# Performance work log

Hardware: AMD Instinct MI355X
Metric: run time of the kernel (lower is better)

## Reference

```python
import jax, jax.numpy as jnp
import numpy as np

D_IN = 768
D_OUT = 768
NUM_HEADS = 12
HEAD_DIM = D_OUT // NUM_HEADS


def setup_inputs() -> dict:
    key = jax.random.key(0)
    ks = jax.random.split(key, 6)
    s = 0.02
    x = jax.random.normal(ks[0], (4, 1024, D_IN), dtype=jnp.float32)
    # torch Linear weights are [out_features, in_features]
    Wq = jax.random.normal(ks[1], (D_OUT, D_IN), dtype=jnp.float32) * s
    Wk = jax.random.normal(ks[2], (D_OUT, D_IN), dtype=jnp.float32) * s
    Wv = jax.random.normal(ks[3], (D_OUT, D_IN), dtype=jnp.float32) * s
    Wo = jax.random.normal(ks[4], (D_OUT, D_OUT), dtype=jnp.float32) * s
    bo = jax.random.normal(ks[5], (D_OUT,), dtype=jnp.float32) * s
    return {"x": x, "Wq": Wq, "Wk": Wk, "Wv": Wv, "Wo": Wo, "bo": bo}


def reference(x, Wq, Wk, Wv, Wo, bo):
    B, T, _ = x.shape
    H, Dh = NUM_HEADS, HEAD_DIM
    # QKV projections (no bias), reshape to [B, H, T, Dh]
    q = (x @ Wq.T).reshape(B, T, H, Dh).transpose(0, 2, 1, 3)
    k = (x @ Wk.T).reshape(B, T, H, Dh).transpose(0, 2, 1, 3)
    v = (x @ Wv.T).reshape(B, T, H, Dh).transpose(0, 2, 1, 3)
    # Scores [B, H, T, T]. NOTE: original torch code's masked_fill and dropout
    # are not in-place / not assigned, so neither affects the output.
    scores = jnp.einsum("bhqd,bhkd->bhqk", q, k)
    attn = jax.nn.softmax(scores / np.sqrt(Dh).astype(np.float32), axis=-1)
    ctx = jnp.einsum("bhqk,bhkd->bhqd", attn, v)
    ctx = ctx.transpose(0, 2, 1, 3).reshape(B, T, H * Dh)
    return ctx @ Wo.T + bo
```

## Files before the change

### kernel.cpp

```cpp
#include <hip/hip_runtime.h>

typedef _Float16 half8 __attribute__((ext_vector_type(8)));
typedef float f32x4 __attribute__((ext_vector_type(4)));
typedef unsigned short u16;

#define NHEAD 12
#define DHEAD 64
#define DM    768
#define TSEQ  1024

static constexpr size_t OFF_XH  = 0;
static constexpr size_t OFF_WQH = 3145728;
static constexpr size_t OFF_WKH = 3735552;
static constexpr size_t OFF_WVH = 4325376;
static constexpr size_t OFF_WOH = 4915200;
static constexpr size_t OFF_Q   = 5505024;
static constexpr size_t OFF_K   = 8650752;
static constexpr size_t OFF_VT  = 11796480;
static constexpr size_t OFF_CTX = 0;

typedef const __attribute__((address_space(1))) void* gas_ptr;
typedef __attribute__((address_space(3))) void* las_ptr;
__device__ __forceinline__ void gload16(const _Float16* g, _Float16* l) {
    __builtin_amdgcn_global_load_lds((gas_ptr)g, (las_ptr)l, 16, 0, 0);
}

__global__ void cvt_kernel(const float* __restrict__ x, const float* __restrict__ wq,
                           const float* __restrict__ wk, const float* __restrict__ wv,
                           const float* __restrict__ wo, _Float16* __restrict__ ws) {
    int seg = blockIdx.y;
    const float* src;
    _Float16* dst;
    int n;
    if (seg == 0)      { src = x;  dst = ws + OFF_XH;  n = 3145728; }
    else if (seg == 1) { src = wq; dst = ws + OFF_WQH; n = 589824; }
    else if (seg == 2) { src = wk; dst = ws + OFF_WKH; n = 589824; }
    else if (seg == 3) { src = wv; dst = ws + OFF_WVH; n = 589824; }
    else               { src = wo; dst = ws + OFF_WOH; n = 589824; }
    int i = (blockIdx.x * blockDim.x + threadIdx.x) * 8;
    if (i < n) {
        float4 v0 = *(const float4*)(src + i);
        float4 v1 = *(const float4*)(src + i + 4);
        half8 o;
        o[0] = (_Float16)v0.x; o[1] = (_Float16)v0.y;
        o[2] = (_Float16)v0.z; o[3] = (_Float16)v0.w;
        o[4] = (_Float16)v1.x; o[5] = (_Float16)v1.y;
        o[6] = (_Float16)v1.z; o[7] = (_Float16)v1.w;
        *(half8*)(dst + i) = o;
    }
}

__global__ __launch_bounds__(256) void qkv_kernel(_Float16* __restrict__ ws) {
    __shared__ __align__(16) _Float16 ldsA[128 * 32];
    __shared__ __align__(16) _Float16 ldsB[128 * 32];

    const int z = blockIdx.z;
    const _Float16* __restrict__ xh = ws + OFF_XH;
    const _Float16* __restrict__ w  = ws + (z == 0 ? OFF_WQH : z == 1 ? OFF_WKH : OFF_WVH);
    _Float16* __restrict__ outp     = ws + (z == 0 ? OFF_Q   : z == 1 ? OFF_K   : OFF_VT);

    const int tid  = threadIdx.x;
    const int lane = tid & 63;
    const int wid  = tid >> 6;
    const int quad = lane >> 4, l15 = lane & 15;
    const int wm = (wid & 1) * 64, wn = (wid >> 1) * 64;

    int mb, nb;
    const _Float16 *gA, *gB;
    if (z < 2) {
        mb = blockIdx.x * 128;
        nb = blockIdx.y * 128;
        gA = xh + (size_t)mb * DM;
        gB = w  + (size_t)nb * DM;
    } else {
        mb = blockIdx.y * 128;
        nb = blockIdx.x * 128;
        gA = w  + (size_t)mb * DM;
        gB = xh + (size_t)nb * DM;
    }

    const int srow = (lane >> 2);
    const int scol = (lane & 3) * 8;
    const size_t goff0 = (size_t)(wid * 32 + srow) * DM + scol;
    const size_t goff1 = (size_t)(wid * 32 + 16 + srow) * DM + scol;
    _Float16* lA0 = ldsA + wid * 1024;
    _Float16* lA1 = ldsA + wid * 1024 + 512;
    _Float16* lB0 = ldsB + wid * 1024;
    _Float16* lB1 = ldsB + wid * 1024 + 512;

    f32x4 acc[4][4] = {};
    for (int k0 = 0; k0 < DM; k0 += 32) {
        gload16(gA + goff0 + k0, lA0);
        gload16(gA + goff1 + k0, lA1);
        gload16(gB + goff0 + k0, lB0);
        gload16(gB + goff1 + k0, lB1);
        __syncthreads();

        half8 a[4], b[4];
#pragma unroll
        for (int t = 0; t < 4; t++) {
            a[t] = *(const half8*)(ldsA + (wm + t * 16 + l15) * 32 + quad * 8);
            b[t] = *(const half8*)(ldsB + (wn + t * 16 + l15) * 32 + quad * 8);
        }
#pragma unroll
        for (int mt = 0; mt < 4; mt++)
#pragma unroll
            for (int nt = 0; nt < 4; nt++)
                acc[mt][nt] = __builtin_amdgcn_mfma_f32_16x16x32_f16(a[mt], b[nt], acc[mt][nt], 0, 0, 0);
        __syncthreads();
    }

#pragma unroll
    for (int mt = 0; mt < 4; mt++)
#pragma unroll
        for (int nt = 0; nt < 4; nt++)
#pragma unroll
            for (int r = 0; r < 4; r++) {
                int m = mb + wm + mt * 16 + quad * 4 + r;
                int n = nb + wn + nt * 16 + l15;
                size_t idx;
                if (z < 2) {
                    int bb = m >> 10, tt = m & 1023;
                    int h = n >> 6, d = n & 63;
                    idx = ((size_t)(bb * NHEAD + h) * TSEQ + tt) * DHEAD + d;
                } else {
                    int h = m >> 6, d = m & 63;
                    int bb = n >> 10, tt = n & 1023;
                    idx = ((size_t)(bb * NHEAD + h) * DHEAD + d) * TSEQ + tt;
                }
                outp[idx] = (_Float16)acc[mt][nt][r];
            }
}

__global__ __launch_bounds__(256, 3) void attn_kernel(_Float16* __restrict__ ws) {
    __shared__ __align__(16) _Float16 ldsK[64 * 64];
    __shared__ __align__(16) _Float16 ldsV[64 * 64];
    __shared__ __align__(16) _Float16 ldsP[4][16 * 72];

    const int tid  = threadIdx.x;
    const int lane = tid & 63;
    const int wid  = tid >> 6;
    const int quad = lane >> 4, l15 = lane & 15;
    const int bh = blockIdx.y;
    const int q0 = blockIdx.x * 64 + wid * 16;

    const _Float16* __restrict__ Q  = ws + OFF_Q  + (size_t)bh * TSEQ * DHEAD;
    const _Float16* __restrict__ K  = ws + OFF_K  + (size_t)bh * TSEQ * DHEAD;
    const _Float16* __restrict__ VT = ws + OFF_VT + (size_t)bh * DHEAD * TSEQ;
    _Float16* __restrict__ ctx = ws + OFF_CTX;
    _Float16* pbase = ldsP[wid];

    const int srow0 = tid >> 3, sc0 = tid & 7;
    const int ldsOff0 = srow0 * 64 + ((sc0 ^ (srow0 & 7)) * 8);
    const int ldsOff1 = (srow0 + 32) * 64 + ((sc0 ^ (srow0 & 7)) * 8);

    half8 qf[2];
#pragma unroll
    for (int ks = 0; ks < 2; ks++)
        qf[ks] = *(const half8*)(Q + (size_t)(q0 + l15) * DHEAD + ks * 32 + quad * 8);

    float mrun[4], lrun[4];
    f32x4 oacc[4] = {};
#pragma unroll
    for (int r = 0; r < 4; r++) { mrun[r] = -1e30f; lrun[r] = 0.f; }

    uint4 ka, kb, va, vb;
    ka = *(const uint4*)(K + tid * 8);
    kb = *(const uint4*)(K + 2048 + tid * 8);
    va = *(const uint4*)(VT + (size_t)srow0 * TSEQ + sc0 * 8);
    vb = *(const uint4*)(VT + (size_t)(srow0 + 32) * TSEQ + sc0 * 8);

    for (int kt = 0; kt < TSEQ; kt += 64) {
        *(uint4*)(ldsK + ldsOff0) = ka;
        *(uint4*)(ldsK + ldsOff1) = kb;
        *(uint4*)(ldsV + ldsOff0) = va;
        *(uint4*)(ldsV + ldsOff1) = vb;
        __syncthreads();

        if (kt + 64 < TSEQ) {
            ka = *(const uint4*)(K + (kt + 64) * DHEAD + tid * 8);
            kb = *(const uint4*)(K + (kt + 64) * DHEAD + 2048 + tid * 8);
            va = *(const uint4*)(VT + (size_t)srow0 * TSEQ + kt + 64 + sc0 * 8);
            vb = *(const uint4*)(VT + (size_t)(srow0 + 32) * TSEQ + kt + 64 + sc0 * 8);
        }

        half8 kf[4][2];
#pragma unroll
        for (int n = 0; n < 4; n++)
#pragma unroll
            for (int ks = 0; ks < 2; ks++) {
                int row = n * 16 + l15;
                int phys = (ks * 4 + quad) ^ (row & 7);
                kf[n][ks] = *(const half8*)(ldsK + row * 64 + phys * 8);
            }

        f32x4 s[4] = {};
#pragma unroll
        for (int n = 0; n < 4; n++)
#pragma unroll
            for (int ks = 0; ks < 2; ks++)
                s[n] = __builtin_amdgcn_mfma_f32_16x16x32_f16(qf[ks], kf[n][ks], s[n], 0, 0, 0);
#pragma unroll
        for (int n = 0; n < 4; n++) s[n] *= 0.125f;

#pragma unroll
        for (int r = 0; r < 4; r++) {
            float tm = fmaxf(fmaxf(s[0][r], s[1][r]), fmaxf(s[2][r], s[3][r]));
#pragma unroll
            for (int off = 1; off < 16; off <<= 1) tm = fmaxf(tm, __shfl_xor(tm, off, 64));
            float mnew = fmaxf(mrun[r], tm);
            float alpha = __expf(mrun[r] - mnew);
            mrun[r] = mnew;
            float ts = 0.f;
#pragma unroll
            for (int n = 0; n < 4; n++) {
                float e = __expf(s[n][r] - mnew);
                s[n][r] = e;
                ts += e;
            }
#pragma unroll
            for (int off = 1; off < 16; off <<= 1) ts += __shfl_xor(ts, off, 64);
            lrun[r] = lrun[r] * alpha + ts;
#pragma unroll
            for (int dn = 0; dn < 4; dn++) oacc[dn][r] *= alpha;
        }

#pragma unroll
        for (int n = 0; n < 4; n++)
#pragma unroll
            for (int r = 0; r < 4; r++)
                pbase[(quad * 4 + r) * 72 + n * 16 + l15] = (_Float16)s[n][r];

        half8 vf[4][2];
#pragma unroll
        for (int dn = 0; dn < 4; dn++)
#pragma unroll
            for (int ks = 0; ks < 2; ks++) {
                int row = dn * 16 + l15;
                int phys = (ks * 4 + quad) ^ (row & 7);
                vf[dn][ks] = *(const half8*)(ldsV + row * 64 + phys * 8);
            }

        half8 pf[2];
#pragma unroll
        for (int ks = 0; ks < 2; ks++)
            pf[ks] = *(const half8*)(pbase + l15 * 72 + ks * 32 + quad * 8);

#pragma unroll
        for (int dn = 0; dn < 4; dn++)
#pragma unroll
            for (int ks = 0; ks < 2; ks++)
                oacc[dn] = __builtin_amdgcn_mfma_f32_16x16x32_f16(pf[ks], vf[dn][ks], oacc[dn], 0, 0, 0);

        __syncthreads();
    }

    const int b_ = bh / NHEAD, h = bh % NHEAD;
#pragma unroll
    for (int dn = 0; dn < 4; dn++)
#pragma unroll
        for (int r = 0; r < 4; r++) {
            int t_ = q0 + quad * 4 + r;
            int col = h * DHEAD + dn * 16 + l15;
            float v = oacc[dn][r] / lrun[r];
            ctx[((size_t)(b_ * TSEQ + t_)) * DM + col] = (_Float16)v;
        }
}

__global__ __launch_bounds__(256) void proj_kernel(const _Float16* __restrict__ ws,
                                                   const float* __restrict__ bo,
                                                   float* __restrict__ out) {
    __shared__ __align__(16) _Float16 ldsA[128 * 32];
    __shared__ __align__(16) _Float16 ldsB[128 * 32];

    const _Float16* __restrict__ gA = ws + OFF_CTX + (size_t)blockIdx.x * 128 * DM;
    const _Float16* __restrict__ gB = ws + OFF_WOH + (size_t)blockIdx.y * 128 * DM;

    const int tid  = threadIdx.x;
    const int lane = tid & 63;
    const int wid  = tid >> 6;
    const int quad = lane >> 4, l15 = lane & 15;
    const int wm = (wid & 1) * 64, wn = (wid >> 1) * 64;

    const int srow = (lane >> 2);
    const int scol = (lane & 3) * 8;
    const size_t goff0 = (size_t)(wid * 32 + srow) * DM + scol;
    const size_t goff1 = (size_t)(wid * 32 + 16 + srow) * DM + scol;
    _Float16* lA0 = ldsA + wid * 1024;
    _Float16* lA1 = ldsA + wid * 1024 + 512;
    _Float16* lB0 = ldsB + wid * 1024;
    _Float16* lB1 = ldsB + wid * 1024 + 512;

    f32x4 acc[4][4] = {};
    for (int k0 = 0; k0 < DM; k0 += 32) {
        gload16(gA + goff0 + k0, lA0);
        gload16(gA + goff1 + k0, lA1);
        gload16(gB + goff0 + k0, lB0);
        gload16(gB + goff1 + k0, lB1);
        __syncthreads();

        half8 a[4], b[4];
#pragma unroll
        for (int t = 0; t < 4; t++) {
            a[t] = *(const half8*)(ldsA + (wm + t * 16 + l15) * 32 + quad * 8);
            b[t] = *(const half8*)(ldsB + (wn + t * 16 + l15) * 32 + quad * 8);
        }
#pragma unroll
        for (int mt = 0; mt < 4; mt++)
#pragma unroll
            for (int nt = 0; nt < 4; nt++)
                acc[mt][nt] = __builtin_amdgcn_mfma_f32_16x16x32_f16(a[mt], b[nt], acc[mt][nt], 0, 0, 0);
        __syncthreads();
    }

    const int mb = blockIdx.x * 128, nb = blockIdx.y * 128;
#pragma unroll
    for (int mt = 0; mt < 4; mt++)
#pragma unroll
        for (int nt = 0; nt < 4; nt++)
#pragma unroll
            for (int r = 0; r < 4; r++) {
                int m = mb + wm + mt * 16 + quad * 4 + r;
                int n = nb + wn + nt * 16 + l15;
                out[(size_t)m * DM + n] = acc[mt][nt][r] + bo[n];
            }
}

extern "C" void kernel_launch(void* const* d_in, const int* in_sizes, int n_in,
                              void* d_out, int out_size, void* d_ws, size_t ws_size,
                              hipStream_t stream) {
    const float* x  = (const float*)d_in[0];
    const float* wq = (const float*)d_in[1];
    const float* wk = (const float*)d_in[2];
    const float* wv = (const float*)d_in[3];
    const float* wo = (const float*)d_in[4];
    const float* bo = (const float*)d_in[5];
    _Float16* ws = (_Float16*)d_ws;
    float* out = (float*)d_out;

    cvt_kernel<<<dim3(1536, 5, 1), 256, 0, stream>>>(x, wq, wk, wv, wo, ws);
    qkv_kernel<<<dim3(32, 6, 3), 256, 0, stream>>>(ws);
    attn_kernel<<<dim3(16, 48, 1), 256, 0, stream>>>(ws);
    proj_kernel<<<dim3(32, 6, 1), 256, 0, stream>>>(ws, bo, out);
}
```

Baseline: 160.8 us.

## Split attention over the key dimension with a combine kernel, use exp2 softmax

Adds a split-K flash-attention path that divides the 1024 keys into two halves across blockIdx.z. It writes unnormalized fp16 partial outputs plus per-row max and sum to the workspace, and a new combine kernel merges them into ctx. This doubles the grid to raise occupancy and parallelism (768 to 1536 blocks), at the cost of an extra launch and extra global traffic. It also folds the 1/sqrt(d) scale into Q in fp16 and replaces __expf with exp2 plus an FMA. The split path runs only when the workspace is large enough.

```diff
diff --git a/kernel.cpp b/kernel.cpp
--- a/kernel.cpp
+++ b/kernel.cpp
@@ -8,6 +8,7 @@
 #define DHEAD 64
 #define DM    768
 #define TSEQ  1024
+#define LOG2E 1.44269504f
 
 static constexpr size_t OFF_XH  = 0;
 static constexpr size_t OFF_WQH = 3145728;
@@ -18,6 +19,9 @@
 static constexpr size_t OFF_K   = 8650752;
 static constexpr size_t OFF_VT  = 11796480;
 static constexpr size_t OFF_CTX = 0;
+static constexpr size_t OFF_OP  = 14942208;
+static constexpr size_t OFF_ML_BYTES = 42467328;
+static constexpr size_t WS_NEED_SPLITK = 43253760;
 
 typedef const __attribute__((address_space(1))) void* gas_ptr;
 typedef __attribute__((address_space(3))) void* las_ptr;
@@ -132,7 +136,8 @@
             }
 }
 
-__global__ __launch_bounds__(256, 3) void attn_kernel(_Float16* __restrict__ ws) {
+template <int NZ>
+__device__ __forceinline__ void attn_body(_Float16* __restrict__ ws) {
     __shared__ __align__(16) _Float16 ldsK[64 * 64];
     __shared__ __align__(16) _Float16 ldsV[64 * 64];
     __shared__ __align__(16) _Float16 ldsP[4][16 * 72];
@@ -142,12 +147,13 @@
     const int wid  = tid >> 6;
     const int quad = lane >> 4, l15 = lane & 15;
     const int bh = blockIdx.y;
+    const int z  = (NZ > 1) ? blockIdx.z : 0;
     const int q0 = blockIdx.x * 64 + wid * 16;
+    const int kbeg = z * (TSEQ / NZ), kend = kbeg + TSEQ / NZ;
 
     const _Float16* __restrict__ Q  = ws + OFF_Q  + (size_t)bh * TSEQ * DHEAD;
     const _Float16* __restrict__ K  = ws + OFF_K  + (size_t)bh * TSEQ * DHEAD;
     const _Float16* __restrict__ VT = ws + OFF_VT + (size_t)bh * DHEAD * TSEQ;
-    _Float16* __restrict__ ctx = ws + OFF_CTX;
     _Float16* pbase = ldsP[wid];
 
     const int srow0 = tid >> 3, sc0 = tid & 7;
@@ -156,8 +162,10 @@
 
     half8 qf[2];
 #pragma unroll
-    for (int ks = 0; ks < 2; ks++)
+    for (int ks = 0; ks < 2; ks++) {
         qf[ks] = *(const half8*)(Q + (size_t)(q0 + l15) * DHEAD + ks * 32 + quad * 8);
+        qf[ks] = qf[ks] * (_Float16)0.125f;
+    }
 
     float mrun[4], lrun[4];
     f32x4 oacc[4] = {};
@@ -165,19 +173,19 @@
     for (int r = 0; r < 4; r++) { mrun[r] = -1e30f; lrun[r] = 0.f; }
 
     uint4 ka, kb, va, vb;
-    ka = *(const uint4*)(K + tid * 8);
-    kb = *(const uint4*)(K + 2048 + tid * 8);
-    va = *(const uint4*)(VT + (size_t)srow0 * TSEQ + sc0 * 8);
-    vb = *(const uint4*)(VT + (size_t)(srow0 + 32) * TSEQ + sc0 * 8);
-
-    for (int kt = 0; kt < TSEQ; kt += 64) {
+    ka = *(const uint4*)(K + kbeg * DHEAD + tid * 8);
+    kb = *(const uint4*)(K + kbeg * DHEAD + 2048 + tid * 8);
+    va = *(const uint4*)(VT + (size_t)srow0 * TSEQ + kbeg + sc0 * 8);
+    vb = *(const uint4*)(VT + (size_t)(srow0 + 32) * TSEQ + kbeg + sc0 * 8);
+
+    for (int kt = kbeg; kt < kend; kt += 64) {
         *(uint4*)(ldsK + ldsOff0) = ka;
         *(uint4*)(ldsK + ldsOff1) = kb;
         *(uint4*)(ldsV + ldsOff0) = va;
         *(uint4*)(ldsV + ldsOff1) = vb;
         __syncthreads();
 
-        if (kt + 64 < TSEQ) {
+        if (kt + 64 < kend) {
             ka = *(const uint4*)(K + (kt + 64) * DHEAD + tid * 8);
             kb = *(const uint4*)(K + (kt + 64) * DHEAD + 2048 + tid * 8);
             va = *(const uint4*)(VT + (size_t)srow0 * TSEQ + kt + 64 + sc0 * 8);
@@ -200,8 +208,6 @@
 #pragma unroll
             for (int ks = 0; ks < 2; ks++)
                 s[n] = __builtin_amdgcn_mfma_f32_16x16x32_f16(qf[ks], kf[n][ks], s[n], 0, 0, 0);
-#pragma unroll
-        for (int n = 0; n < 4; n++) s[n] *= 0.125f;
 
 #pragma unroll
         for (int r = 0; r < 4; r++) {
@@ -209,18 +215,19 @@
 #pragma unroll
             for (int off = 1; off < 16; off <<= 1) tm = fmaxf(tm, __shfl_xor(tm, off, 64));
             float mnew = fmaxf(mrun[r], tm);
-            float alpha = __expf(mrun[r] - mnew);
+            float alpha = __builtin_amdgcn_exp2f((mrun[r] - mnew) * LOG2E);
             mrun[r] = mnew;
+            float mL = mnew * LOG2E;
             float ts = 0.f;
 #pragma unroll
             for (int n = 0; n < 4; n++) {
-                float e = __expf(s[n][r] - mnew);
+                float e = __builtin_amdgcn_exp2f(__builtin_fmaf(s[n][r], LOG2E, -mL));
                 s[n][r] = e;
                 ts += e;
             }
 #pragma unroll
             for (int off = 1; off < 16; off <<= 1) ts += __shfl_xor(ts, off, 64);
-            lrun[r] = lrun[r] * alpha + ts;
+            lrun[r] = __builtin_fmaf(lrun[r], alpha, ts);
 #pragma unroll
             for (int dn = 0; dn < 4; dn++) oacc[dn][r] *= alpha;
         }
@@ -255,16 +262,71 @@
         __syncthreads();
     }
 
-    const int b_ = bh / NHEAD, h = bh % NHEAD;
-#pragma unroll
-    for (int dn = 0; dn < 4; dn++)
-#pragma unroll
-        for (int r = 0; r < 4; r++) {
-            int t_ = q0 + quad * 4 + r;
-            int col = h * DHEAD + dn * 16 + l15;
-            float v = oacc[dn][r] / lrun[r];
-            ctx[((size_t)(b_ * TSEQ + t_)) * DM + col] = (_Float16)v;
+    if (NZ == 1) {
+        _Float16* __restrict__ ctx = ws + OFF_CTX;
+        const int b_ = bh / NHEAD, h = bh % NHEAD;
+#pragma unroll
+        for (int dn = 0; dn < 4; dn++)
+#pragma unroll
+            for (int r = 0; r < 4; r++) {
+                int t_ = q0 + quad * 4 + r;
+                int col = h * DHEAD + dn * 16 + l15;
+                float v = oacc[dn][r] / lrun[r];
+                ctx[((size_t)(b_ * TSEQ + t_)) * DM + col] = (_Float16)v;
+            }
+    } else {
+        _Float16* __restrict__ op = ws + OFF_OP;
+        float* __restrict__ ml = (float*)((char*)ws + OFF_ML_BYTES);
+        const size_t rowbase = (size_t)z * 48 * TSEQ + (size_t)bh * TSEQ + q0;
+#pragma unroll
+        for (int dn = 0; dn < 4; dn++)
+#pragma unroll
+            for (int r = 0; r < 4; r++) {
+                size_t row = rowbase + quad * 4 + r;
+                op[row * 64 + dn * 16 + l15] = (_Float16)oacc[dn][r];
+            }
+        if (l15 == 0) {
+#pragma unroll
+            for (int r = 0; r < 4; r++) {
+                size_t row = rowbase + quad * 4 + r;
+                ml[row * 2]     = mrun[r];
+                ml[row * 2 + 1] = lrun[r];
+            }
         }
+    }
+}
+
+__global__ __launch_bounds__(256, 3) void attn_kernel(_Float16* __restrict__ ws) {
+    attn_body<1>(ws);
+}
+__global__ __launch_bounds__(256, 6) void attn_splitk_kernel(_Float16* __restrict__ ws) {
+    attn_body<2>(ws);
+}
+
+__global__ __launch_bounds__(256) void combine_kernel(_Float16* __restrict__ ws) {
+    const _Float16* __restrict__ op = ws + OFF_OP;
+    const float* __restrict__ ml = (const float*)((const char*)ws + OFF_ML_BYTES);
+    _Float16* __restrict__ ctx = ws + OFF_CTX;
+
+    int g = blockIdx.x * 256 + threadIdx.x;
+    int row = g >> 3, chunk = g & 7;
+    int bh = row >> 10, q = row & 1023;
+    int b_ = bh / NHEAD, h = bh % NHEAD;
+
+    float m0 = ml[(size_t)row * 2], l0 = ml[(size_t)row * 2 + 1];
+    float m1 = ml[(size_t)(49152 + row) * 2], l1 = ml[(size_t)(49152 + row) * 2 + 1];
+    float M = fmaxf(m0, m1);
+    float w0 = __builtin_amdgcn_exp2f((m0 - M) * LOG2E);
+    float w1 = __builtin_amdgcn_exp2f((m1 - M) * LOG2E);
+    float inv_l = 1.0f / (w0 * l0 + w1 * l1);
+
+    half8 o0 = *(const half8*)(op + (size_t)row * 64 + chunk * 8);
+    half8 o1 = *(const half8*)(op + (size_t)(49152 + row) * 64 + chunk * 8);
+    half8 o;
+#pragma unroll
+    for (int j = 0; j < 8; j++)
+        o[j] = (_Float16)(((float)o0[j] * w0 + (float)o1[j] * w1) * inv_l);
+    *(half8*)(ctx + ((size_t)(b_ * TSEQ + q)) * DM + h * DHEAD + chunk * 8) = o;
 }
 
 __global__ __launch_bounds__(256) void proj_kernel(const _Float16* __restrict__ ws,
@@ -340,6 +402,11 @@
 
     cvt_kernel<<<dim3(1536, 5, 1), 256, 0, stream>>>(x, wq, wk, wv, wo, ws);
     qkv_kernel<<<dim3(32, 6, 3), 256, 0, stream>>>(ws);
-    attn_kernel<<<dim3(16, 48, 1), 256, 0, stream>>>(ws);
+    if (ws_size >= WS_NEED_SPLITK) {
+        attn_splitk_kernel<<<dim3(16, 48, 2), 256, 0, stream>>>(ws);
+        combine_kernel<<<dim3(1536, 1, 1), 256, 0, stream>>>(ws);
+    } else {
+        attn_kernel<<<dim3(16, 48, 1), 256, 0, stream>>>(ws);
+    }
     proj_kernel<<<dim3(32, 6, 1), 256, 0, stream>>>(ws, bo, out);
 }
```

After: 215.0 us. +33.6%, slower.
